# Optimization experiments

Measured on AMD Instinct MI355X. Metric: run time of the kernel, lower is better.

The kernel has to match this reference:

```python
import jax, jax.numpy as jnp
import numpy as np

D = 1024
H = 16
HD = D // H
FF = 4 * D
EPS = 1e-5


def _layernorm(x, scale, shift):
    # Faithful to the torch module: unbiased std (ddof=1), eps added to std.
    mean = jnp.mean(x, axis=-1, keepdims=True)
    var = jnp.sum((x - mean) ** 2, axis=-1, keepdims=True) / (x.shape[-1] - 1)
    std = jnp.sqrt(var)
    return shift + scale * (x - mean) / (std + EPS)


def _gelu(x):
    c = jnp.sqrt(jnp.asarray(2.0 / jnp.pi, dtype=x.dtype))
    return 0.5 * x * (1.0 + jnp.tanh(c * (x + 0.044715 * x ** 3)))


def setup_inputs() -> dict:
    key = jax.random.key(0)
    ks = jax.random.split(key, 8)
    B, S = 2, 2048
    inv = 1.0 / np.sqrt(D)
    x = jax.random.normal(ks[0], (B, S, D), dtype=jnp.float32)
    scale1 = jnp.ones((D,), jnp.float32)
    shift1 = jnp.zeros((D,), jnp.float32)
    Wqkv = jax.random.normal(ks[1], (3 * D, D), jnp.float32) * inv  # torch layout [out,in]
    Wo_w = jax.random.normal(ks[2], (D, D), jnp.float32) * inv
    Wo_b = jnp.zeros((D,), jnp.float32)
    scale2 = jnp.ones((D,), jnp.float32)
    shift2 = jnp.zeros((D,), jnp.float32)
    W1 = jax.random.normal(ks[3], (FF, D), jnp.float32) * inv
    b1 = jnp.zeros((FF,), jnp.float32)
    W2 = jax.random.normal(ks[4], (D, FF), jnp.float32) * (1.0 / np.sqrt(FF))
    b2 = jnp.zeros((D,), jnp.float32)
    return {"x": x, "scale1": scale1, "shift1": shift1, "Wqkv": Wqkv,
            "Wo_w": Wo_w, "Wo_b": Wo_b, "scale2": scale2, "shift2": shift2,
            "W1": W1, "b1": b1, "W2": W2, "b2": b2}


def reference(x, scale1, shift1, Wqkv, Wo_w, Wo_b, scale2, shift2, W1, b1, W2, b2):
    B, S, _ = x.shape
    # --- pre-norm attention ---
    h = _layernorm(x, scale1, shift1)
    qkv = jnp.einsum('bsd,ed->bse', h, Wqkv)  # [B,S,3D]
    q, k, v = jnp.split(qkv, 3, axis=-1)
    q = q.reshape(B, S, H, HD).transpose(0, 2, 1, 3)  # [B,H,S,HD]
    k = k.reshape(B, S, H, HD).transpose(0, 2, 1, 3)
    v = v.reshape(B, S, H, HD).transpose(0, 2, 1, 3)
    scores = jnp.einsum('bhqd,bhkd->bhqk', q, k) / jnp.sqrt(jnp.asarray(HD, x.dtype))
    causal = jnp.triu(jnp.ones((S, S), dtype=bool), k=1)
    scores = jnp.where(causal, -jnp.inf, scores)
    weights = jax.nn.softmax(scores, axis=-1)
    attn = jnp.einsum('bhqk,bhkd->bhqd', weights, v)
    attn = attn.transpose(0, 2, 1, 3).reshape(B, S, D)
    attn = jnp.einsum('bsd,ed->bse', attn, Wo_w) + Wo_b
    x = x + attn
    # --- pre-norm MLP ---
    h2 = _layernorm(x, scale2, shift2)
    m = _gelu(jnp.einsum('bsd,fd->bsf', h2, W1) + b1)
    m = jnp.einsum('bsf,df->bsd', m, W2) + b2
    return x + m
```

## Files before the change

kernel.cpp:

```cpp
#include <hip/hip_runtime.h>
#include <cstdint>
#include <cstddef>

typedef __bf16 bf16;
typedef __bf16 v8bf __attribute__((ext_vector_type(8)));
typedef __bf16 v4bf __attribute__((ext_vector_type(4)));
typedef float  v4f  __attribute__((ext_vector_type(4)));

#define D_MODEL 1024
#define FF_DIM  4096
#define SEQ     2048
#define NTOK    4096
#define NH      16
#define HDIM    64

#define GLOAD_LDS16(g, l) \
    __builtin_amdgcn_global_load_lds((const __attribute__((address_space(1))) void*)(g), \
                                     (__attribute__((address_space(3))) void*)(l), 16, 0, 0)

#define QSCALE 0.18033688011112042f
#define SHIFT2 -28.853900817779268f

__global__ __launch_bounds__(256) void prep_kernel(
    const float* __restrict__ Wqkv, const float* __restrict__ Wo,
    const float* __restrict__ W1, const float* __restrict__ W2,
    bf16* __restrict__ Wqkv_b, bf16* __restrict__ Wo_b,
    bf16* __restrict__ W1_b, bf16* __restrict__ W2_b) {
    int u = blockIdx.x * 256 + threadIdx.x;
    const float* src; bf16* dst; int idx;
    if (u < 786432)       { src = Wqkv; dst = Wqkv_b; idx = u * 4; }
    else if (u < 1048576) { src = Wo;   dst = Wo_b;   idx = (u - 786432) * 4; }
    else if (u < 2097152) { src = W1;   dst = W1_b;   idx = (u - 1048576) * 4; }
    else                  { src = W2;   dst = W2_b;   idx = (u - 2097152) * 4; }
    float4 v = *(const float4*)(src + idx);
    dst[idx + 0] = (bf16)v.x;
    dst[idx + 1] = (bf16)v.y;
    dst[idx + 2] = (bf16)v.z;
    dst[idx + 3] = (bf16)v.w;
}

__global__ __launch_bounds__(256) void layernorm_kernel(
    const float* __restrict__ x, const float* __restrict__ scale,
    const float* __restrict__ shift, bf16* __restrict__ out) {
    int row = blockIdx.x;
    int t = threadIdx.x;
    const float* xr = x + (size_t)row * D_MODEL;
    float4 v = *(const float4*)(xr + t * 4);
    float s  = v.x + v.y + v.z + v.w;
    float sq = v.x * v.x + v.y * v.y + v.z * v.z + v.w * v.w;
    #pragma unroll
    for (int o = 1; o < 64; o <<= 1) {
        s  += __shfl_xor(s, o);
        sq += __shfl_xor(sq, o);
    }
    __shared__ float ws[8];
    int wv = t >> 6;
    if ((t & 63) == 0) { ws[wv * 2] = s; ws[wv * 2 + 1] = sq; }
    __syncthreads();
    s  = ws[0] + ws[2] + ws[4] + ws[6];
    sq = ws[1] + ws[3] + ws[5] + ws[7];
    float mean = s * (1.0f / D_MODEL);
    float var  = (sq - (float)D_MODEL * mean * mean) * (1.0f / (D_MODEL - 1));
    var = fmaxf(var, 0.0f);
    float inv = 1.0f / (sqrtf(var) + 1e-5f);
    #pragma unroll
    for (int j = 0; j < 4; ++j) {
        int c = t * 4 + j;
        float xv = (&v.x)[j];
        out[(size_t)row * D_MODEL + c] = (bf16)(shift[c] + scale[c] * (xv - mean) * inv);
    }
}

__global__ __launch_bounds__(256) void transpose_v(
    const bf16* __restrict__ vb, bf16* __restrict__ vt) {
    int bh = blockIdx.x >> 5;
    int ts = blockIdx.x & 31;
    int t = threadIdx.x;
    __shared__ bf16 T[64][72];
    const bf16* src = vb + ((size_t)bh * SEQ + ts * 64) * HDIM;
    #pragma unroll
    for (int half = 0; half < 2; ++half) {
        int s = (t >> 3) + half * 32;
        int d0 = (t & 7) * 8;
        v8bf vv = *(const v8bf*)(src + (size_t)s * HDIM + d0);
        #pragma unroll
        for (int j = 0; j < 8; ++j) T[d0 + j][s] = vv[j];
    }
    __syncthreads();
    bf16* dst = vt + (size_t)bh * HDIM * SEQ + ts * 64;
    int d = t >> 2;
    #pragma unroll
    for (int cc = 0; cc < 2; ++cc) {
        int c = (t & 3) + cc * 4;
        v8bf o = *(const v8bf*)(&T[d][c * 8]);
        *(v8bf*)(dst + (size_t)d * SEQ + c * 8) = o;
    }
}

template <int EPI>
__global__ __launch_bounds__(256) void gemm_nt(
    const bf16* __restrict__ A, const bf16* __restrict__ Bw,
    const float* __restrict__ bias, const float* __restrict__ resid,
    float* __restrict__ outf, bf16* __restrict__ ob0,
    bf16* __restrict__ ob1, bf16* __restrict__ ob2,
    int M, int N, int K, int klen) {
    __shared__ __align__(16) bf16 As[128 * 64];
    __shared__ __align__(16) bf16 Bs[128 * 64];
    int gx = gridDim.x;
    int lin = blockIdx.y * gx + blockIdx.x;
    int grpsz = 16 * gx;
    int group = lin / grpsz;
    int rem = lin - group * grpsz;
    int m_t = group * 16 + (rem & 15);
    int n_t = rem >> 4;
    int m0 = m_t * 128, n0 = n_t * 128;
    int kstart = blockIdx.z * klen;
    int t = threadIdx.x;
    int lane = t & 63, wave = t >> 6;
    int wm = wave >> 1, wn = wave & 1;
    int quad = lane >> 4, l16 = lane & 15;

    int srow8 = lane >> 3;
    int schunk = (lane & 7) ^ srow8;
    const bf16* agp = A  + (size_t)(m0 + wave * 8 + srow8) * K + kstart + schunk * 8;
    const bf16* bgp = Bw + (size_t)(n0 + wave * 8 + srow8) * K + kstart + schunk * 8;
    size_t row32 = (size_t)32 * K;

    v4f acc[4][4];
    #pragma unroll
    for (int i = 0; i < 4; ++i)
        #pragma unroll
        for (int j = 0; j < 4; ++j)
            acc[i][j] = (v4f){0.f, 0.f, 0.f, 0.f};

    int rsw = l16 & 7;
    for (int kk = 0; kk < klen; kk += 64) {
        __syncthreads();
        #pragma unroll
        for (int ii = 0; ii < 4; ++ii) {
            GLOAD_LDS16(agp + ii * row32 + kk, &As[ii * 2048 + wave * 512]);
            GLOAD_LDS16(bgp + ii * row32 + kk, &Bs[ii * 2048 + wave * 512]);
        }
        __syncthreads();
        #pragma unroll
        for (int h = 0; h < 2; ++h) {
            v8bf af[4], bfr[4];
            #pragma unroll
            for (int i = 0; i < 4; ++i)
                af[i] = *(const v8bf*)(&As[(wm * 64 + i * 16 + l16) * 64 + (((h * 4 + quad) ^ rsw)) * 8]);
            #pragma unroll
            for (int j = 0; j < 4; ++j)
                bfr[j] = *(const v8bf*)(&Bs[(wn * 64 + j * 16 + l16) * 64 + (((h * 4 + quad) ^ rsw)) * 8]);
            #pragma unroll
            for (int i = 0; i < 4; ++i)
                #pragma unroll
                for (int j = 0; j < 4; ++j)
                    acc[i][j] = __builtin_amdgcn_mfma_f32_16x16x32_bf16(af[i], bfr[j], acc[i][j], 0, 0, 0);
        }
    }

    #pragma unroll
    for (int i = 0; i < 4; ++i) {
        #pragma unroll
        for (int j = 0; j < 4; ++j) {
            #pragma unroll
            for (int r = 0; r < 4; ++r) {
                float v = acc[i][j][r];
                int row = m0 + wm * 64 + i * 16 + quad * 4 + r;
                int col = n0 + wn * 64 + j * 16 + l16;
                if (EPI == 0) {
                    int which = col >> 10, rr = col & 1023;
                    int h = rr >> 6, d = rr & 63;
                    int b = row >> 11, sI = row & 2047;
                    size_t dst = (((size_t)(b * NH + h)) * SEQ + sI) * HDIM + d;
                    if (which == 0)      ob0[dst] = (bf16)(v * QSCALE);
                    else if (which == 1) ob1[dst] = (bf16)v;
                    else                 ob2[dst] = (bf16)v;
                } else if (EPI == 1) {
                    size_t o = (size_t)row * N + col;
                    outf[o] = resid[o] + v + bias[col];
                } else if (EPI == 2) {
                    float u = v + bias[col];
                    float y = 1.5957691216057308f * (u + 0.044715f * u * u * u);
                    float g = u * __builtin_amdgcn_rcpf(1.0f + __expf(-y));
                    ob0[(size_t)row * N + col] = (bf16)g;
                } else {
                    ob0[(size_t)blockIdx.z * M * N + (size_t)row * N + col] = (bf16)v;
                }
            }
        }
    }
}

__global__ __launch_bounds__(256) void combine_w2(
    const bf16* __restrict__ part, const float* __restrict__ x1,
    const float* __restrict__ b2, float* __restrict__ out) {
    int i = (blockIdx.x * 256 + threadIdx.x) * 4;
    int col = i & (D_MODEL - 1);
    float4 xv = *(const float4*)(x1 + i);
    float4 bv = *(const float4*)(b2 + col);
    float4 r;
    r.x = xv.x + bv.x; r.y = xv.y + bv.y; r.z = xv.z + bv.z; r.w = xv.w + bv.w;
    #pragma unroll
    for (int z = 0; z < 4; ++z) {
        v4bf p = *(const v4bf*)(part + (size_t)z * NTOK * D_MODEL + i);
        r.x += (float)p[0]; r.y += (float)p[1]; r.z += (float)p[2]; r.w += (float)p[3];
    }
    *(float4*)(out + i) = r;
}

__device__ __forceinline__ void attn_process_tile(
    int kv, int qwb, int quad, int l16,
    const bf16* Ks, const bf16* Vs, bf16* Pw,
    const v8bf& qf0, const v8bf& qf1, v4f (&o)[4], float& lsum) {
    #pragma unroll
    for (int hh = 0; hh < 2; ++hh) {
        int kb32 = kv + hh * 32;
        if (kb32 > qwb + 15) break;
        #pragma unroll
        for (int j2 = 0; j2 < 2; ++j2) {
            int j = hh * 2 + j2;
            int kb16 = kb32 + j2 * 16;
            union { bf16 h[4]; uint2 u; } pk;
            if (kb16 > qwb + 15) {
                pk.u = (uint2){0u, 0u};
            } else {
                int key = j * 16 + l16;
                v8bf ka = *(const v8bf*)(&Ks[(key * 8 + (quad ^ (key & 7))) * 8]);
                v8bf kc = *(const v8bf*)(&Ks[(key * 8 + ((quad + 4) ^ (key & 7))) * 8]);
                v4f s = (v4f){SHIFT2, SHIFT2, SHIFT2, SHIFT2};
                s = __builtin_amdgcn_mfma_f32_16x16x32_bf16(ka, qf0, s, 0, 0, 0);
                s = __builtin_amdgcn_mfma_f32_16x16x32_bf16(kc, qf1, s, 0, 0, 0);
                bool dm = (kb16 + 15 > qwb);
                int keyb = kb16 + quad * 4;
                #pragma unroll
                for (int r = 0; r < 4; ++r) {
                    float pv = __builtin_amdgcn_exp2f(s[r]);
                    if (dm) pv = (keyb + r <= qwb + l16) ? pv : 0.f;
                    lsum += pv;
                    pk.h[r] = (bf16)pv;
                }
            }
            *(uint2*)(&Pw[l16 * 80 + j * 16 + quad * 4]) = pk.u;
        }
        v8bf pf = *(const v8bf*)(&Pw[l16 * 80 + hh * 32 + quad * 8]);
        #pragma unroll
        for (int dc = 0; dc < 4; ++dc) {
            int dim = dc * 16 + l16;
            v8bf vv = *(const v8bf*)(&Vs[(dim * 8 + ((quad + 4 * hh) ^ (dim & 7))) * 8]);
            o[dc] = __builtin_amdgcn_mfma_f32_16x16x32_bf16(pf, vv, o[dc], 0, 0, 0);
        }
    }
}

__global__ __launch_bounds__(256) void attn_kernel(
    const bf16* __restrict__ qb, const bf16* __restrict__ kb,
    const bf16* __restrict__ vt, bf16* __restrict__ ob) {
    int bh = blockIdx.x & 31;
    int pr = blockIdx.x >> 5;
    int qtA = pr, qtB = 31 - pr;

    int t = threadIdx.x;
    int wave = t >> 6, lane = t & 63;
    int quad = lane >> 4, l16 = lane & 15;
    int qwbA = qtA * 64 + wave * 16;
    int qwbB = qtB * 64 + wave * 16;

    const bf16* Qh  = qb + (size_t)bh * SEQ * HDIM;
    const bf16* Kh  = kb + (size_t)bh * SEQ * HDIM;
    const bf16* Vth = vt + (size_t)bh * HDIM * SEQ;

    __shared__ __align__(16) bf16 Ks[64 * 64];
    __shared__ __align__(16) bf16 Vs[64 * 64];
    __shared__ __align__(16) bf16 Ps[4][16 * 80];
    bf16* Pw = &Ps[wave][0];

    int u0 = t, u1 = t + 256;
    int key0 = u0 >> 3, c0 = (u0 & 7) ^ (key0 & 7);
    int key1 = u1 >> 3, c1 = (u1 & 7) ^ (key1 & 7);
    bf16* kdst0 = &Ks[wave * 512];
    bf16* kdst1 = &Ks[2048 + wave * 512];
    bf16* vdst0 = &Vs[wave * 512];
    bf16* vdst1 = &Vs[2048 + wave * 512];
    const bf16* Ksrc0 = Kh + (size_t)key0 * HDIM + c0 * 8;
    const bf16* Ksrc1 = Kh + (size_t)key1 * HDIM + c1 * 8;
    const bf16* Vsrc0 = Vth + (size_t)key0 * SEQ + c0 * 8;
    const bf16* Vsrc1 = Vth + (size_t)key1 * SEQ + c1 * 8;

    v8bf qfA0 = *(const v8bf*)(Qh + (size_t)(qwbA + l16) * HDIM + quad * 8);
    v8bf qfA1 = *(const v8bf*)(Qh + (size_t)(qwbA + l16) * HDIM + 32 + quad * 8);
    v8bf qfB0 = *(const v8bf*)(Qh + (size_t)(qwbB + l16) * HDIM + quad * 8);
    v8bf qfB1 = *(const v8bf*)(Qh + (size_t)(qwbB + l16) * HDIM + 32 + quad * 8);

    v4f oA[4], oB[4];
    #pragma unroll
    for (int dc = 0; dc < 4; ++dc) {
        oA[dc] = (v4f){0.f, 0.f, 0.f, 0.f};
        oB[dc] = (v4f){0.f, 0.f, 0.f, 0.f};
    }
    float lA = 0.f, lB = 0.f;

    int kvendA = qtA * 64 + 64;
    int kvendB = qtB * 64 + 64;
    for (int kv = 0; kv < kvendB; kv += 64) {
        __syncthreads();
        GLOAD_LDS16(Ksrc0 + (size_t)kv * HDIM, kdst0);
        GLOAD_LDS16(Ksrc1 + (size_t)kv * HDIM, kdst1);
        GLOAD_LDS16(Vsrc0 + kv, vdst0);
        GLOAD_LDS16(Vsrc1 + kv, vdst1);
        __syncthreads();
        if (kv < kvendA)
            attn_process_tile(kv, qwbA, quad, l16, Ks, Vs, Pw, qfA0, qfA1, oA, lA);
        attn_process_tile(kv, qwbB, quad, l16, Ks, Vs, Pw, qfB0, qfB1, oB, lB);
    }

    lA += __shfl_xor(lA, 16); lA += __shfl_xor(lA, 32);
    lB += __shfl_xor(lB, 16); lB += __shfl_xor(lB, 32);

    int b = bh >> 4, h = bh & 15;
    #pragma unroll
    for (int r = 0; r < 4; ++r) {
        float invA = 1.0f / __shfl(lA, quad * 4 + r);
        float invB = 1.0f / __shfl(lB, quad * 4 + r);
        int sA = qwbA + quad * 4 + r;
        int sB = qwbB + quad * 4 + r;
        #pragma unroll
        for (int dc = 0; dc < 4; ++dc) {
            int d = dc * 16 + l16;
            ob[((size_t)(b * SEQ + sA)) * D_MODEL + h * HDIM + d] = (bf16)(oA[dc][r] * invA);
            ob[((size_t)(b * SEQ + sB)) * D_MODEL + h * HDIM + d] = (bf16)(oB[dc][r] * invB);
        }
    }
}

extern "C" void kernel_launch(void* const* d_in, const int* in_sizes, int n_in,
                              void* d_out, int out_size, void* d_ws, size_t ws_size,
                              hipStream_t stream) {
    const float* x      = (const float*)d_in[0];
    const float* scale1 = (const float*)d_in[1];
    const float* shift1 = (const float*)d_in[2];
    const float* Wqkv   = (const float*)d_in[3];
    const float* Wo_w   = (const float*)d_in[4];
    const float* Wo_b   = (const float*)d_in[5];
    const float* scale2 = (const float*)d_in[6];
    const float* shift2 = (const float*)d_in[7];
    const float* W1     = (const float*)d_in[8];
    const float* b1     = (const float*)d_in[9];
    const float* W2     = (const float*)d_in[10];
    const float* b2     = (const float*)d_in[11];
    float* out = (float*)d_out;

    char* ws = (char*)d_ws;
    size_t off = 0;
    auto alloc = [&](size_t bytes) -> char* {
        char* p = ws + off;
        off += (bytes + 255) & ~(size_t)255;
        return p;
    };
    bf16* Wqkv_b = (bf16*)alloc((size_t)3 * D_MODEL * D_MODEL * 2);
    bf16* Wo_bf  = (bf16*)alloc((size_t)D_MODEL * D_MODEL * 2);
    bf16* W1_b   = (bf16*)alloc((size_t)FF_DIM * D_MODEL * 2);
    bf16* W2_b   = (bf16*)alloc((size_t)D_MODEL * FF_DIM * 2);
    bf16* bufA   = (bf16*)alloc((size_t)NTOK * D_MODEL * 2);
    bf16* qb     = (bf16*)alloc((size_t)NTOK * D_MODEL * 2);
    bf16* kb     = (bf16*)alloc((size_t)NTOK * D_MODEL * 2);
    bf16* vb     = (bf16*)alloc((size_t)NTOK * D_MODEL * 2);
    bf16* vtb    = (bf16*)alloc((size_t)NTOK * D_MODEL * 2);
    float* x1    = (float*)alloc((size_t)NTOK * D_MODEL * 4);
    bf16* mbuf   = (bf16*)alloc((size_t)NTOK * FF_DIM * 2);
    bf16* w2part = bufA;
    (void)ws_size; (void)n_in; (void)in_sizes; (void)out_size;

    prep_kernel<<<12288, 256, 0, stream>>>(Wqkv, Wo_w, W1, W2,
                                           Wqkv_b, Wo_bf, W1_b, W2_b);

    layernorm_kernel<<<NTOK, 256, 0, stream>>>(x, scale1, shift1, bufA);

    gemm_nt<0><<<dim3(3072 / 128, NTOK / 128), 256, 0, stream>>>(
        bufA, Wqkv_b, nullptr, nullptr, nullptr, qb, kb, vb, NTOK, 3072, D_MODEL, D_MODEL);

    transpose_v<<<1024, 256, 0, stream>>>(vb, vtb);

    attn_kernel<<<512, 256, 0, stream>>>(qb, kb, vtb, bufA);

    gemm_nt<1><<<dim3(D_MODEL / 128, NTOK / 128), 256, 0, stream>>>(
        bufA, Wo_bf, Wo_b, x, x1, nullptr, nullptr, nullptr, NTOK, D_MODEL, D_MODEL, D_MODEL);

    layernorm_kernel<<<NTOK, 256, 0, stream>>>(x1, scale2, shift2, qb);

    gemm_nt<2><<<dim3(FF_DIM / 128, NTOK / 128), 256, 0, stream>>>(
        qb, W1_b, b1, nullptr, nullptr, mbuf, nullptr, nullptr, NTOK, FF_DIM, D_MODEL, D_MODEL);

    gemm_nt<6><<<dim3(D_MODEL / 128, NTOK / 128, 4), 256, 0, stream>>>(
        mbuf, W2_b, nullptr, nullptr, nullptr, w2part, nullptr, nullptr, NTOK, D_MODEL, FF_DIM, FF_DIM / 4);

    combine_w2<<<NTOK * D_MODEL / 1024, 256, 0, stream>>>(w2part, x1, b2, out);
}
```

Measured before the change: 340.0 us.

## Switch GEMM to 32x32x16 MFMA and fuse first layernorm into prep kernel

The GEMM inner loop moves from 16x16x32 MFMA tiles (4x4 per wave) to 32x32x16 MFMA tiles (2x2 per wave), with the LDS read indexing and epilogue row/column mapping rewritten to match the 32x32 output layout. This halves the number of MFMA instructions and LDS fragment loads per k-step. Separately, the first layernorm is folded into the weight-conversion prep kernel as extra blocks, saving one kernel launch. The new epilogue mapping has to match the 32x32 accumulator layout exactly.

```diff
diff --git a/kernel.cpp b/kernel.cpp
--- a/kernel.cpp
+++ b/kernel.cpp
@@ -6,6 +6,7 @@
 typedef __bf16 v8bf __attribute__((ext_vector_type(8)));
 typedef __bf16 v4bf __attribute__((ext_vector_type(4)));
 typedef float  v4f  __attribute__((ext_vector_type(4)));
+typedef float  v16f __attribute__((ext_vector_type(16)));
 
 #define D_MODEL 1024
 #define FF_DIM  4096
@@ -25,18 +26,50 @@
     const float* __restrict__ Wqkv, const float* __restrict__ Wo,
     const float* __restrict__ W1, const float* __restrict__ W2,
     bf16* __restrict__ Wqkv_b, bf16* __restrict__ Wo_b,
-    bf16* __restrict__ W1_b, bf16* __restrict__ W2_b) {
-    int u = blockIdx.x * 256 + threadIdx.x;
-    const float* src; bf16* dst; int idx;
-    if (u < 786432)       { src = Wqkv; dst = Wqkv_b; idx = u * 4; }
-    else if (u < 1048576) { src = Wo;   dst = Wo_b;   idx = (u - 786432) * 4; }
-    else if (u < 2097152) { src = W1;   dst = W1_b;   idx = (u - 1048576) * 4; }
-    else                  { src = W2;   dst = W2_b;   idx = (u - 2097152) * 4; }
-    float4 v = *(const float4*)(src + idx);
-    dst[idx + 0] = (bf16)v.x;
-    dst[idx + 1] = (bf16)v.y;
-    dst[idx + 2] = (bf16)v.z;
-    dst[idx + 3] = (bf16)v.w;
+    bf16* __restrict__ W1_b, bf16* __restrict__ W2_b,
+    const float* __restrict__ x, const float* __restrict__ scale1,
+    const float* __restrict__ shift1, bf16* __restrict__ h1) {
+    __shared__ float wsh[8];
+    if (blockIdx.x < 12288) {
+        int u = blockIdx.x * 256 + threadIdx.x;
+        const float* src; bf16* dst; int idx;
+        if (u < 786432)       { src = Wqkv; dst = Wqkv_b; idx = u * 4; }
+        else if (u < 1048576) { src = Wo;   dst = Wo_b;   idx = (u - 786432) * 4; }
+        else if (u < 2097152) { src = W1;   dst = W1_b;   idx = (u - 1048576) * 4; }
+        else                  { src = W2;   dst = W2_b;   idx = (u - 2097152) * 4; }
+        float4 v = *(const float4*)(src + idx);
+        dst[idx + 0] = (bf16)v.x;
+        dst[idx + 1] = (bf16)v.y;
+        dst[idx + 2] = (bf16)v.z;
+        dst[idx + 3] = (bf16)v.w;
+        return;
+    }
+    int row = blockIdx.x - 12288;
+    int t = threadIdx.x;
+    const float* xr = x + (size_t)row * D_MODEL;
+    float4 v = *(const float4*)(xr + t * 4);
+    float s  = v.x + v.y + v.z + v.w;
+    float sq = v.x * v.x + v.y * v.y + v.z * v.z + v.w * v.w;
+    #pragma unroll
+    for (int o = 1; o < 64; o <<= 1) {
+        s  += __shfl_xor(s, o);
+        sq += __shfl_xor(sq, o);
+    }
+    int wv = t >> 6;
+    if ((t & 63) == 0) { wsh[wv * 2] = s; wsh[wv * 2 + 1] = sq; }
+    __syncthreads();
+    s  = wsh[0] + wsh[2] + wsh[4] + wsh[6];
+    sq = wsh[1] + wsh[3] + wsh[5] + wsh[7];
+    float mean = s * (1.0f / D_MODEL);
+    float var  = (sq - (float)D_MODEL * mean * mean) * (1.0f / (D_MODEL - 1));
+    var = fmaxf(var, 0.0f);
+    float inv = 1.0f / (sqrtf(var) + 1e-5f);
+    #pragma unroll
+    for (int j = 0; j < 4; ++j) {
+        int c = t * 4 + j;
+        float xv = (&v.x)[j];
+        h1[(size_t)row * D_MODEL + c] = (bf16)(shift1[c] + scale1[c] * (xv - mean) * inv);
+    }
 }
 
 __global__ __launch_bounds__(256) void layernorm_kernel(
@@ -118,7 +151,7 @@
     int t = threadIdx.x;
     int lane = t & 63, wave = t >> 6;
     int wm = wave >> 1, wn = wave & 1;
-    int quad = lane >> 4, l16 = lane & 15;
+    int l31 = lane & 31, hi = lane >> 5;
 
     int srow8 = lane >> 3;
     int schunk = (lane & 7) ^ srow8;
@@ -126,14 +159,16 @@
     const bf16* bgp = Bw + (size_t)(n0 + wave * 8 + srow8) * K + kstart + schunk * 8;
     size_t row32 = (size_t)32 * K;
 
-    v4f acc[4][4];
-    #pragma unroll
-    for (int i = 0; i < 4; ++i)
-        #pragma unroll
-        for (int j = 0; j < 4; ++j)
-            acc[i][j] = (v4f){0.f, 0.f, 0.f, 0.f};
-
-    int rsw = l16 & 7;
+    v16f acc[2][2];
+    #pragma unroll
+    for (int i = 0; i < 2; ++i)
+        #pragma unroll
+        for (int j = 0; j < 2; ++j)
+            #pragma unroll
+            for (int r = 0; r < 16; ++r)
+                acc[i][j][r] = 0.f;
+
+    int rsw = l31 & 7;
     for (int kk = 0; kk < klen; kk += 64) {
         __syncthreads();
         #pragma unroll
@@ -143,31 +178,32 @@
         }
         __syncthreads();
         #pragma unroll
-        for (int h = 0; h < 2; ++h) {
-            v8bf af[4], bfr[4];
+        for (int h = 0; h < 4; ++h) {
+            int chunk = h * 2 + hi;
+            v8bf af[2], bfr[2];
             #pragma unroll
-            for (int i = 0; i < 4; ++i)
-                af[i] = *(const v8bf*)(&As[(wm * 64 + i * 16 + l16) * 64 + (((h * 4 + quad) ^ rsw)) * 8]);
+            for (int i = 0; i < 2; ++i)
+                af[i] = *(const v8bf*)(&As[(wm * 64 + i * 32 + l31) * 64 + (chunk ^ rsw) * 8]);
             #pragma unroll
-            for (int j = 0; j < 4; ++j)
-                bfr[j] = *(const v8bf*)(&Bs[(wn * 64 + j * 16 + l16) * 64 + (((h * 4 + quad) ^ rsw)) * 8]);
+            for (int j = 0; j < 2; ++j)
+                bfr[j] = *(const v8bf*)(&Bs[(wn * 64 + j * 32 + l31) * 64 + (chunk ^ rsw) * 8]);
             #pragma unroll
-            for (int i = 0; i < 4; ++i)
+            for (int i = 0; i < 2; ++i)
                 #pragma unroll
-                for (int j = 0; j < 4; ++j)
-                    acc[i][j] = __builtin_amdgcn_mfma_f32_16x16x32_bf16(af[i], bfr[j], acc[i][j], 0, 0, 0);
-        }
-    }
-
-    #pragma unroll
-    for (int i = 0; i < 4; ++i) {
-        #pragma unroll
-        for (int j = 0; j < 4; ++j) {
+                for (int j = 0; j < 2; ++j)
+                    acc[i][j] = __builtin_amdgcn_mfma_f32_32x32x16_bf16(af[i], bfr[j], acc[i][j], 0, 0, 0);
+        }
+    }
+
+    #pragma unroll
+    for (int i = 0; i < 2; ++i) {
+        #pragma unroll
+        for (int j = 0; j < 2; ++j) {
             #pragma unroll
-            for (int r = 0; r < 4; ++r) {
-                float v = acc[i][j][r];
-                int row = m0 + wm * 64 + i * 16 + quad * 4 + r;
-                int col = n0 + wn * 64 + j * 16 + l16;
+            for (int reg = 0; reg < 16; ++reg) {
+                float v = acc[i][j][reg];
+                int row = m0 + wm * 64 + i * 32 + (reg & 3) + 8 * (reg >> 2) + 4 * hi;
+                int col = n0 + wn * 64 + j * 32 + l31;
                 if (EPI == 0) {
                     int which = col >> 10, rr = col & 1023;
                     int h = rr >> 6, d = rr & 63;
@@ -371,10 +407,9 @@
     bf16* w2part = bufA;
     (void)ws_size; (void)n_in; (void)in_sizes; (void)out_size;
 
-    prep_kernel<<<12288, 256, 0, stream>>>(Wqkv, Wo_w, W1, W2,
-                                           Wqkv_b, Wo_bf, W1_b, W2_b);
-
-    layernorm_kernel<<<NTOK, 256, 0, stream>>>(x, scale1, shift1, bufA);
+    prep_kernel<<<16384, 256, 0, stream>>>(Wqkv, Wo_w, W1, W2,
+                                           Wqkv_b, Wo_bf, W1_b, W2_b,
+                                           x, scale1, shift1, bufA);
 
     gemm_nt<0><<<dim3(3072 / 128, NTOK / 128), 256, 0, stream>>>(
         bufA, Wqkv_b, nullptr, nullptr, nullptr, qb, kb, vb, NTOK, 3072, D_MODEL, D_MODEL);
```

Result: no change. 341.6 us (+0.5%).
